# Optimization experiments

Hardware: AMD Instinct MI355X
Metric: run time of the kernel (lower is better)

Reference implementation:

```python
import jax, jax.numpy as jnp
import numpy as np


def setup_inputs() -> dict:
    key = jax.random.key(0)
    ks = jax.random.split(key, 7)
    B, I, H = 8192, 1024, 1024
    x = jax.random.normal(ks[0], (B, I), dtype=jnp.float32)
    h_prev = jax.random.normal(ks[1], (B, H), dtype=jnp.float32)
    C_prev = jax.random.normal(ks[2], (B, H), dtype=jnp.float32)
    W_f = jax.random.normal(ks[3], (I + H, H), dtype=jnp.float32) * 0.01
    W_i = jax.random.normal(ks[4], (I + H, H), dtype=jnp.float32) * 0.01
    W_C = jax.random.normal(ks[5], (I + H, H), dtype=jnp.float32) * 0.01
    W_o = jax.random.normal(ks[6], (I + H, H), dtype=jnp.float32) * 0.01
    b = jnp.zeros((H,), dtype=jnp.float32)
    return {"x": x, "h_prev": h_prev, "C_prev": C_prev,
            "W_f": W_f, "b_f": b, "W_i": W_i, "b_i": b,
            "W_C": W_C, "b_C": b, "W_o": W_o, "b_o": b}


def reference(x, h_prev, C_prev, W_f, b_f, W_i, b_i, W_C, b_C, W_o, b_o):
    combined = jnp.concatenate([x, h_prev], axis=1)  # [B, I+H]
    # Fuse the four gate GEMMs into one [B, I+H] x [I+H, 4H] matmul.
    W = jnp.concatenate([W_f, W_i, W_o, W_C], axis=1)  # [I+H, 4H]
    b = jnp.concatenate([b_f, b_i, b_o, b_C], axis=0)  # [4H]
    gates = combined @ W + b                            # [B, 4H]
    H = C_prev.shape[1]
    f_t = jax.nn.sigmoid(gates[:, 0:H])
    i_t = jax.nn.sigmoid(gates[:, H:2 * H])
    o_t = jax.nn.sigmoid(gates[:, 2 * H:3 * H])
    C_tilda = jnp.tanh(gates[:, 3 * H:4 * H])
    C_t = f_t * C_prev + i_t * C_tilda
    h_t = o_t * jnp.tanh(C_t)
    return (h_t, C_t)
```

## Files before the change

### kernel.cpp

```cpp
#include <hip/hip_runtime.h>
#include <hip/hip_bf16.h>

#define B_SZ 8192
#define IH   2048
#define H_SZ 1024
#define BM   256
#define BK   32
#define NKT  (IH / BK)
#define DB2  32768
#define WOF  16384

typedef __attribute__((ext_vector_type(8))) short  short8;
typedef __attribute__((ext_vector_type(4))) float  floatx4;

static __device__ __forceinline__ ushort f2bf(float f) {
  union { float f; unsigned u; } v; v.f = f;
  unsigned u = v.u;
  u += 0x7fffu + ((u >> 16) & 1u);
  return (ushort)(u >> 16);
}
static __device__ __forceinline__ float sigmoidf_(float x) {
  return 1.0f / (1.0f + __expf(-x));
}
static __device__ __forceinline__ float tanhf_(float x) {
  float ax = fabsf(x);
  float e = __expf(-2.0f * ax);
  float t = (1.0f - e) / (1.0f + e);
  return copysignf(t, x);
}
static __device__ __forceinline__ void gload_lds16(const void* gsrc, void* ldst) {
  __builtin_amdgcn_global_load_lds(
      (__attribute__((address_space(1))) const void*)gsrc,
      (__attribute__((address_space(3))) void*)ldst, 16, 0, 0);
}

__global__ __launch_bounds__(256) void convert_w_kernel(
    const float* __restrict__ Wf, const float* __restrict__ Wi,
    const float* __restrict__ Wo, const float* __restrict__ Wc,
    ushort* __restrict__ Wt) {
  __shared__ float tile[64][65];
  const int g  = blockIdx.z;
  const float* W = (g == 0) ? Wf : (g == 1) ? Wi : (g == 2) ? Wo : Wc;
  const int n0 = blockIdx.x * 64;
  const int k0 = blockIdx.y * 64;
  const int tid = threadIdx.x;
#pragma unroll
  for (int i = 0; i < 4; ++i) {
    int c = i * 256 + tid;
    int r = c >> 4, c4 = c & 15;
    float4 v = *(const float4*)(W + (size_t)(k0 + r) * H_SZ + n0 + c4 * 4);
    tile[r][c4 * 4 + 0] = v.x;
    tile[r][c4 * 4 + 1] = v.y;
    tile[r][c4 * 4 + 2] = v.z;
    tile[r][c4 * 4 + 3] = v.w;
  }
  __syncthreads();
  const int n  = tid >> 2;
  const int kc = (tid & 3) * 16;
  ushort o[16] __attribute__((aligned(16)));
#pragma unroll
  for (int e = 0; e < 16; ++e) o[e] = f2bf(tile[kc + e][n]);
  ushort* dst = Wt + ((size_t)g * H_SZ + n0 + n) * IH + k0 + kc;
  *(uint4*)(dst)     = *(uint4*)&o[0];
  *(uint4*)(dst + 8) = *(uint4*)&o[8];
}

__global__ __launch_bounds__(256) void convert_a_kernel(
    const float* __restrict__ x, const float* __restrict__ hp,
    ushort* __restrict__ Abf) {
  size_t idx = ((size_t)blockIdx.x * 256 + threadIdx.x) * 8;
  size_t row = idx >> 11;
  size_t col = idx & 2047;
  const float* src = (col < 1024) ? (x  + row * 1024 + col)
                                  : (hp + row * 1024 + (col - 1024));
  float4 v0 = *(const float4*)(src);
  float4 v1 = *(const float4*)(src + 4);
  ushort o[8] __attribute__((aligned(16)));
  o[0] = f2bf(v0.x); o[1] = f2bf(v0.y); o[2] = f2bf(v0.z); o[3] = f2bf(v0.w);
  o[4] = f2bf(v1.x); o[5] = f2bf(v1.y); o[6] = f2bf(v1.z); o[7] = f2bf(v1.w);
  *(uint4*)(Abf + idx) = *(uint4*)&o[0];
}

__global__ __launch_bounds__(512, 2) void lstm_fused_kernel(
    const float* __restrict__ Cp, const ushort* __restrict__ Wt,
    const ushort* __restrict__ Abf,
    const float* __restrict__ bf_, const float* __restrict__ bi_,
    const float* __restrict__ bo_, const float* __restrict__ bc_,
    float* __restrict__ out) {
  __shared__ char lds[2 * DB2];

  const int bid = blockIdx.x;
  const int wg  = (bid & 7) * 64 + (bid >> 3);
  const int b0  = (wg >> 4) * BM;
  const int n0g = (wg & 15) * 64;

  const int tid = threadIdx.x;
  const int ln  = tid & 63;
  const int wv  = tid >> 6;
  const int wm  = wv >> 1, wn = wv & 1;

  floatx4 acc[4][8];
#pragma unroll
  for (int m = 0; m < 4; ++m)
#pragma unroll
    for (int j = 0; j < 8; ++j) acc[m][j] = {0.f, 0.f, 0.f, 0.f};

  const int q  = ((ln & 15) >> 1) & 3;
  const int sx = ((ln >> 4) ^ q) << 4;
  const int aB = (wm * 64 + (ln & 15)) * 64 + sx;
  const int bB = WOF + (wn * 32 + (ln & 15)) * 64 + sx;

  const unsigned kg = ((unsigned)(tid & 3)) ^ ((unsigned)(tid >> 3) & 3);
  const char* AbfB = (const char*)Abf;
  const char* WtB  = (const char*)Wt;
  unsigned aoff[2], woff[2];
#pragma unroll
  for (int i = 0; i < 2; ++i) {
    int row = i * 128 + (tid >> 2);
    aoff[i] = (unsigned)(b0 + row) * 4096u + kg * 16u;
    int gate = row >> 6, nloc = row & 63;
    woff[i] = (unsigned)(gate * 1024 + n0g + nloc) * 4096u + kg * 16u;
  }
  const int dst0 = wv * 1024;

#define STAGE(db, ktb)                                                        \
  do {                                                                        \
    gload_lds16(AbfB + (aoff[0] + (unsigned)(ktb)), lds + (db) + dst0);       \
    gload_lds16(AbfB + (aoff[1] + (unsigned)(ktb)), lds + (db) + 8192 + dst0);\
    gload_lds16(WtB  + (woff[0] + (unsigned)(ktb)), lds + (db) + WOF + dst0); \
    gload_lds16(WtB  + (woff[1] + (unsigned)(ktb)), lds + (db) + WOF + 8192 + dst0);\
  } while (0)

  short8 aFA[4], bFA[8];
  short8 aFB[4], bFB[8];
#define RDSET(AF, BF, db)                                                     \
  do {                                                                        \
    _Pragma("unroll")                                                         \
    for (int mf_ = 0; mf_ < 4; ++mf_)                                         \
      AF[mf_] = *(const short8*)(lds + (db) + aB + mf_ * 1024);               \
    _Pragma("unroll")                                                         \
    for (int j_ = 0; j_ < 8; ++j_)                                            \
      BF[j_] = *(const short8*)(lds + (db) + bB + (j_ >> 1) * 4096 +          \
                                (j_ & 1) * 1024);                             \
  } while (0)
#define MFALL(AF, BF)                                                         \
  do {                                                                        \
    __builtin_amdgcn_s_setprio(1);                                            \
    _Pragma("unroll")                                                         \
    for (int mf_ = 0; mf_ < 4; ++mf_)                                         \
      _Pragma("unroll")                                                       \
      for (int j_ = 0; j_ < 8; ++j_)                                          \
        acc[mf_][j_] = __builtin_amdgcn_mfma_f32_16x16x32_bf16(               \
            AF[mf_], BF[j_], acc[mf_][j_], 0, 0, 0);                          \
    __builtin_amdgcn_s_setprio(0);                                            \
  } while (0)
#define BAR    __builtin_amdgcn_s_barrier()
#define LGKM0  asm volatile("s_waitcnt lgkmcnt(0)" ::: "memory")
#define VMC0   asm volatile("s_waitcnt vmcnt(0)" ::: "memory")

  STAGE(0, 0);
  STAGE(DB2, 64);
  VMC0; BAR;
  RDSET(aFA, bFA, 0);
  LGKM0; BAR;

#pragma unroll 1
  for (int it = 0; it < NKT / 2; ++it) {
    {
      const int ktb = (((2 * it + 2) & 63)) * 64;
      RDSET(aFB, bFB, DB2);
      STAGE(0, ktb);
      MFALL(aFA, bFA);
      LGKM0; VMC0; BAR;
    }
    {
      const int ktb = (((2 * it + 3) & 63)) * 64;
      RDSET(aFA, bFA, 0);
      STAGE(DB2, ktb);
      MFALL(aFB, bFB);
      LGKM0; VMC0; BAR;
    }
  }

  const int colq = ln & 15;
  const int rq   = ln >> 4;
  float* outh = out;
  float* outC = out + (size_t)B_SZ * H_SZ;
#pragma unroll
  for (int mf = 0; mf < 4; ++mf) {
#pragma unroll
    for (int ns = 0; ns < 2; ++ns) {
      int n = n0g + wn * 32 + ns * 16 + colq;
      float vbf = bf_[n], vbi = bi_[n], vbo = bo_[n], vbc = bc_[n];
#pragma unroll
      for (int r = 0; r < 4; ++r) {
        int row = b0 + wm * 64 + mf * 16 + rq * 4 + r;
        float fg = sigmoidf_(acc[mf][0 + ns][r] + vbf);
        float ig = sigmoidf_(acc[mf][2 + ns][r] + vbi);
        float og = sigmoidf_(acc[mf][4 + ns][r] + vbo);
        float cg = tanhf_  (acc[mf][6 + ns][r] + vbc);
        float cp = Cp[(size_t)row * H_SZ + n];
        float Ct = fg * cp + ig * cg;
        float ht = og * tanhf_(Ct);
        outh[(size_t)row * H_SZ + n] = ht;
        outC[(size_t)row * H_SZ + n] = Ct;
      }
    }
  }
#undef STAGE
#undef RDSET
#undef MFALL
#undef BAR
#undef LGKM0
#undef VMC0
}

extern "C" void kernel_launch(void* const* d_in, const int* in_sizes, int n_in,
                              void* d_out, int out_size, void* d_ws, size_t ws_size,
                              hipStream_t stream) {
  const float* x  = (const float*)d_in[0];
  const float* hp = (const float*)d_in[1];
  const float* Cp = (const float*)d_in[2];
  const float* Wf = (const float*)d_in[3];
  const float* bf = (const float*)d_in[4];
  const float* Wi = (const float*)d_in[5];
  const float* bi = (const float*)d_in[6];
  const float* Wc = (const float*)d_in[7];
  const float* bc = (const float*)d_in[8];
  const float* Wo = (const float*)d_in[9];
  const float* bo = (const float*)d_in[10];

  ushort* Wt  = (ushort*)d_ws;
  ushort* Abf = (ushort*)((char*)d_ws + (16u << 20));

  dim3 gridT(16, 32, 4);
  convert_w_kernel<<<gridT, 256, 0, stream>>>(Wf, Wi, Wo, Wc, Wt);
  convert_a_kernel<<<8192, 256, 0, stream>>>(x, hp, Abf);

  lstm_fused_kernel<<<512, 512, 0, stream>>>(Cp, Wt, Abf,
                                             bf, bi, bo, bc, (float*)d_out);
}
```

Baseline: 163.8 us.

## Switch to 32x32x16 MFMA with k-major layouts and direct global A-fragment loads

The activation and weight conversion kernels now write k-chunk-major (8-element groups) layouts, so MFMA fragments can be fetched as contiguous 16-byte vectors. The GEMM kernel moves from 16x16x32 to 32x32x16 bf16 MFMA tiles, which cuts the number of LDS fragment reads per flop. A operands are loaded straight from global memory into registers instead of being staged through LDS, which halves LDS usage to weights only. The trade-off is that A-fragment global latency now sits on the critical path with only a single-step register prefetch, and the activation converter gains a tiled transpose pass.

```diff
diff --git a/kernel.cpp b/kernel.cpp
--- a/kernel.cpp
+++ b/kernel.cpp
@@ -7,11 +7,10 @@
 #define BM   256
 #define BK   32
 #define NKT  (IH / BK)
-#define DB2  32768
-#define WOF  16384
-
-typedef __attribute__((ext_vector_type(8))) short  short8;
-typedef __attribute__((ext_vector_type(4))) float  floatx4;
+#define WBUF 16384
+
+typedef __attribute__((ext_vector_type(8)))  short  short8;
+typedef __attribute__((ext_vector_type(16))) float  floatx16;
 
 static __device__ __forceinline__ ushort f2bf(float f) {
   union { float f; unsigned u; } v; v.f = f;
@@ -34,10 +33,10 @@
       (__attribute__((address_space(3))) void*)ldst, 16, 0, 0);
 }
 
-__global__ __launch_bounds__(256) void convert_w_kernel(
+__global__ __launch_bounds__(256) void convert_w2_kernel(
     const float* __restrict__ Wf, const float* __restrict__ Wi,
     const float* __restrict__ Wo, const float* __restrict__ Wc,
-    ushort* __restrict__ Wt) {
+    ushort* __restrict__ Wt2) {
   __shared__ float tile[64][65];
   const int g  = blockIdx.z;
   const float* W = (g == 0) ? Wf : (g == 1) ? Wi : (g == 2) ? Wo : Wc;
@@ -55,39 +54,59 @@
     tile[r][c4 * 4 + 3] = v.w;
   }
   __syncthreads();
-  const int n  = tid >> 2;
-  const int kc = (tid & 3) * 16;
-  ushort o[16] __attribute__((aligned(16)));
-#pragma unroll
-  for (int e = 0; e < 16; ++e) o[e] = f2bf(tile[kc + e][n]);
-  ushort* dst = Wt + ((size_t)g * H_SZ + n0 + n) * IH + k0 + kc;
-  *(uint4*)(dst)     = *(uint4*)&o[0];
-  *(uint4*)(dst + 8) = *(uint4*)&o[8];
-}
-
-__global__ __launch_bounds__(256) void convert_a_kernel(
+#pragma unroll
+  for (int i = 0; i < 2; ++i) {
+    int u  = i * 256 + tid;
+    int kc = u >> 6;
+    int n  = u & 63;
+    ushort o[8] __attribute__((aligned(16)));
+#pragma unroll
+    for (int e = 0; e < 8; ++e) o[e] = f2bf(tile[kc * 8 + e][n]);
+    ushort* dst = Wt2 + (((size_t)(k0 / 8 + kc) * 4 + g) * 1024 + n0 + n) * 8;
+    *(uint4*)dst = *(uint4*)&o[0];
+  }
+}
+
+__global__ __launch_bounds__(256) void convert_a2_kernel(
     const float* __restrict__ x, const float* __restrict__ hp,
-    ushort* __restrict__ Abf) {
-  size_t idx = ((size_t)blockIdx.x * 256 + threadIdx.x) * 8;
-  size_t row = idx >> 11;
-  size_t col = idx & 2047;
-  const float* src = (col < 1024) ? (x  + row * 1024 + col)
-                                  : (hp + row * 1024 + (col - 1024));
-  float4 v0 = *(const float4*)(src);
-  float4 v1 = *(const float4*)(src + 4);
-  ushort o[8] __attribute__((aligned(16)));
-  o[0] = f2bf(v0.x); o[1] = f2bf(v0.y); o[2] = f2bf(v0.z); o[3] = f2bf(v0.w);
-  o[4] = f2bf(v1.x); o[5] = f2bf(v1.y); o[6] = f2bf(v1.z); o[7] = f2bf(v1.w);
-  *(uint4*)(Abf + idx) = *(uint4*)&o[0];
+    ushort* __restrict__ Abf2) {
+  __shared__ float tile[64][65];
+  const int k0 = blockIdx.x * 64;
+  const int r0 = blockIdx.y * 64;
+  const int tid = threadIdx.x;
+  const float* base = (k0 < 1024) ? x : hp;
+  const int koff = (k0 < 1024) ? k0 : (k0 - 1024);
+#pragma unroll
+  for (int i = 0; i < 4; ++i) {
+    int c = i * 256 + tid;
+    int r = c >> 4, c4 = c & 15;
+    float4 v = *(const float4*)(base + (size_t)(r0 + r) * 1024 + koff + c4 * 4);
+    tile[r][c4 * 4 + 0] = v.x;
+    tile[r][c4 * 4 + 1] = v.y;
+    tile[r][c4 * 4 + 2] = v.z;
+    tile[r][c4 * 4 + 3] = v.w;
+  }
+  __syncthreads();
+#pragma unroll
+  for (int i = 0; i < 2; ++i) {
+    int u  = i * 256 + tid;
+    int kc = u >> 6;
+    int r  = u & 63;
+    ushort o[8] __attribute__((aligned(16)));
+#pragma unroll
+    for (int e = 0; e < 8; ++e) o[e] = f2bf(tile[r][kc * 8 + e]);
+    ushort* dst = Abf2 + ((size_t)(k0 / 8 + kc) * 8192 + r0 + r) * 8;
+    *(uint4*)dst = *(uint4*)&o[0];
+  }
 }
 
 __global__ __launch_bounds__(512, 2) void lstm_fused_kernel(
-    const float* __restrict__ Cp, const ushort* __restrict__ Wt,
-    const ushort* __restrict__ Abf,
+    const float* __restrict__ Cp, const ushort* __restrict__ Wt2,
+    const ushort* __restrict__ Abf2,
     const float* __restrict__ bf_, const float* __restrict__ bi_,
     const float* __restrict__ bo_, const float* __restrict__ bc_,
     float* __restrict__ out) {
-  __shared__ char lds[2 * DB2];
+  __shared__ char lds[2 * WBUF];
 
   const int bid = blockIdx.x;
   const int wg  = (bid & 7) * 64 + (bid >> 3);
@@ -99,116 +118,127 @@
   const int wv  = tid >> 6;
   const int wm  = wv >> 1, wn = wv & 1;
 
-  floatx4 acc[4][8];
-#pragma unroll
-  for (int m = 0; m < 4; ++m)
-#pragma unroll
-    for (int j = 0; j < 8; ++j) acc[m][j] = {0.f, 0.f, 0.f, 0.f};
-
-  const int q  = ((ln & 15) >> 1) & 3;
-  const int sx = ((ln >> 4) ^ q) << 4;
-  const int aB = (wm * 64 + (ln & 15)) * 64 + sx;
-  const int bB = WOF + (wn * 32 + (ln & 15)) * 64 + sx;
-
-  const unsigned kg = ((unsigned)(tid & 3)) ^ ((unsigned)(tid >> 3) & 3);
-  const char* AbfB = (const char*)Abf;
-  const char* WtB  = (const char*)Wt;
-  unsigned aoff[2], woff[2];
+  floatx16 acc[2][4];
+#pragma unroll
+  for (int m = 0; m < 2; ++m)
+#pragma unroll
+    for (int j = 0; j < 4; ++j)
+#pragma unroll
+      for (int e = 0; e < 16; ++e) acc[m][j][e] = 0.f;
+
+  const char* Abf2B = (const char*)Abf2;
+  const unsigned aG = (unsigned)(ln >> 5) * 131072u +
+                      (unsigned)(b0 + wm * 64 + (ln & 31)) * 16u;
+
+  const int bRB = (ln >> 5) * 4096 + (wn * 32 + (ln & 31)) * 16;
+
+  const char* WtB = (const char*)Wt2;
+  unsigned wS[2];
 #pragma unroll
   for (int i = 0; i < 2; ++i) {
-    int row = i * 128 + (tid >> 2);
-    aoff[i] = (unsigned)(b0 + row) * 4096u + kg * 16u;
-    int gate = row >> 6, nloc = row & 63;
-    woff[i] = (unsigned)(gate * 1024 + n0g + nloc) * 4096u + kg * 16u;
-  }
-  const int dst0 = wv * 1024;
-
-#define STAGE(db, ktb)                                                        \
-  do {                                                                        \
-    gload_lds16(AbfB + (aoff[0] + (unsigned)(ktb)), lds + (db) + dst0);       \
-    gload_lds16(AbfB + (aoff[1] + (unsigned)(ktb)), lds + (db) + 8192 + dst0);\
-    gload_lds16(WtB  + (woff[0] + (unsigned)(ktb)), lds + (db) + WOF + dst0); \
-    gload_lds16(WtB  + (woff[1] + (unsigned)(ktb)), lds + (db) + WOF + 8192 + dst0);\
-  } while (0)
-
-  short8 aFA[4], bFA[8];
-  short8 aFB[4], bFB[8];
-#define RDSET(AF, BF, db)                                                     \
+    int c    = 2 * i + (tid >> 8);
+    int nrt  = tid & 255;
+    wS[i] = (unsigned)c * 65536u + (unsigned)(nrt >> 6) * 16384u +
+            (unsigned)(n0g + (nrt & 63)) * 16u;
+  }
+  const int wdst0 = wv * 1024;
+
+#define STAGE_W(db, ktw)                                                      \
+  do {                                                                        \
+    gload_lds16(WtB + (wS[0] + (unsigned)(ktw)), lds + (db) + wdst0);         \
+    gload_lds16(WtB + (wS[1] + (unsigned)(ktw)), lds + (db) + 8192 + wdst0);  \
+  } while (0)
+
+  short8 aFA[2][2], aFB[2][2];
+  short8 bFA[4][2], bFB[4][2];
+#define LOADA(AF, kta)                                                        \
   do {                                                                        \
     _Pragma("unroll")                                                         \
-    for (int mf_ = 0; mf_ < 4; ++mf_)                                         \
-      AF[mf_] = *(const short8*)(lds + (db) + aB + mf_ * 1024);               \
+    for (int mt_ = 0; mt_ < 2; ++mt_)                                         \
+      _Pragma("unroll")                                                       \
+      for (int ks_ = 0; ks_ < 2; ++ks_)                                       \
+        AF[mt_][ks_] = *(const short8*)(Abf2B + (aG + (unsigned)(kta) +       \
+                         (unsigned)ks_ * 262144u + (unsigned)mt_ * 512u));    \
+  } while (0)
+#define RDSET_B(BF, db)                                                       \
+  do {                                                                        \
     _Pragma("unroll")                                                         \
-    for (int j_ = 0; j_ < 8; ++j_)                                            \
-      BF[j_] = *(const short8*)(lds + (db) + bB + (j_ >> 1) * 4096 +          \
-                                (j_ & 1) * 1024);                             \
+    for (int g_ = 0; g_ < 4; ++g_)                                            \
+      _Pragma("unroll")                                                       \
+      for (int ks_ = 0; ks_ < 2; ++ks_)                                       \
+        BF[g_][ks_] = *(const short8*)(lds + (db) + bRB + ks_ * 8192 +        \
+                                       g_ * 1024);                            \
   } while (0)
 #define MFALL(AF, BF)                                                         \
   do {                                                                        \
     __builtin_amdgcn_s_setprio(1);                                            \
     _Pragma("unroll")                                                         \
-    for (int mf_ = 0; mf_ < 4; ++mf_)                                         \
+    for (int ks_ = 0; ks_ < 2; ++ks_)                                         \
       _Pragma("unroll")                                                       \
-      for (int j_ = 0; j_ < 8; ++j_)                                          \
-        acc[mf_][j_] = __builtin_amdgcn_mfma_f32_16x16x32_bf16(               \
-            AF[mf_], BF[j_], acc[mf_][j_], 0, 0, 0);                          \
+      for (int mt_ = 0; mt_ < 2; ++mt_)                                       \
+        _Pragma("unroll")                                                     \
+        for (int g_ = 0; g_ < 4; ++g_)                                        \
+          acc[mt_][g_] = __builtin_amdgcn_mfma_f32_32x32x16_bf16(             \
+              AF[mt_][ks_], BF[g_][ks_], acc[mt_][g_], 0, 0, 0);              \
     __builtin_amdgcn_s_setprio(0);                                            \
   } while (0)
 #define BAR    __builtin_amdgcn_s_barrier()
 #define LGKM0  asm volatile("s_waitcnt lgkmcnt(0)" ::: "memory")
 #define VMC0   asm volatile("s_waitcnt vmcnt(0)" ::: "memory")
 
-  STAGE(0, 0);
-  STAGE(DB2, 64);
+  STAGE_W(0, 0);
+  STAGE_W(WBUF, 262144);
+  LOADA(aFA, 0);
   VMC0; BAR;
-  RDSET(aFA, bFA, 0);
+  RDSET_B(bFA, 0);
   LGKM0; BAR;
 
 #pragma unroll 1
   for (int it = 0; it < NKT / 2; ++it) {
     {
-      const int ktb = (((2 * it + 2) & 63)) * 64;
-      RDSET(aFB, bFB, DB2);
-      STAGE(0, ktb);
+      const unsigned ktaN = (unsigned)((2 * it + 1) & 63) * 524288u;
+      const unsigned ktwN = (unsigned)((2 * it + 2) & 63) * 262144u;
+      RDSET_B(bFB, WBUF);
+      LOADA(aFB, ktaN);
+      STAGE_W(0, ktwN);
       MFALL(aFA, bFA);
       LGKM0; VMC0; BAR;
     }
     {
-      const int ktb = (((2 * it + 3) & 63)) * 64;
-      RDSET(aFA, bFA, 0);
-      STAGE(DB2, ktb);
+      const unsigned ktaN = (unsigned)((2 * it + 2) & 63) * 524288u;
+      const unsigned ktwN = (unsigned)((2 * it + 3) & 63) * 262144u;
+      RDSET_B(bFA, 0);
+      LOADA(aFA, ktaN);
+      STAGE_W(WBUF, ktwN);
       MFALL(aFB, bFB);
       LGKM0; VMC0; BAR;
     }
   }
 
-  const int colq = ln & 15;
-  const int rq   = ln >> 4;
+  const int n = n0g + wn * 32 + (ln & 31);
+  const float vbf = bf_[n], vbi = bi_[n], vbo = bo_[n], vbc = bc_[n];
+  const int h2 = (ln >> 5) * 4;
   float* outh = out;
   float* outC = out + (size_t)B_SZ * H_SZ;
 #pragma unroll
-  for (int mf = 0; mf < 4; ++mf) {
-#pragma unroll
-    for (int ns = 0; ns < 2; ++ns) {
-      int n = n0g + wn * 32 + ns * 16 + colq;
-      float vbf = bf_[n], vbi = bi_[n], vbo = bo_[n], vbc = bc_[n];
-#pragma unroll
-      for (int r = 0; r < 4; ++r) {
-        int row = b0 + wm * 64 + mf * 16 + rq * 4 + r;
-        float fg = sigmoidf_(acc[mf][0 + ns][r] + vbf);
-        float ig = sigmoidf_(acc[mf][2 + ns][r] + vbi);
-        float og = sigmoidf_(acc[mf][4 + ns][r] + vbo);
-        float cg = tanhf_  (acc[mf][6 + ns][r] + vbc);
-        float cp = Cp[(size_t)row * H_SZ + n];
-        float Ct = fg * cp + ig * cg;
-        float ht = og * tanhf_(Ct);
-        outh[(size_t)row * H_SZ + n] = ht;
-        outC[(size_t)row * H_SZ + n] = Ct;
-      }
+  for (int mt = 0; mt < 2; ++mt) {
+#pragma unroll
+    for (int reg = 0; reg < 16; ++reg) {
+      int row = b0 + wm * 64 + mt * 32 + (reg & 3) + 8 * (reg >> 2) + h2;
+      float fg = sigmoidf_(acc[mt][0][reg] + vbf);
+      float ig = sigmoidf_(acc[mt][1][reg] + vbi);
+      float og = sigmoidf_(acc[mt][2][reg] + vbo);
+      float cg = tanhf_  (acc[mt][3][reg] + vbc);
+      float cp = Cp[(size_t)row * H_SZ + n];
+      float Ct = fg * cp + ig * cg;
+      float ht = og * tanhf_(Ct);
+      outh[(size_t)row * H_SZ + n] = ht;
+      outC[(size_t)row * H_SZ + n] = Ct;
     }
   }
-#undef STAGE
-#undef RDSET
+#undef STAGE_W
+#undef LOADA
+#undef RDSET_B
 #undef MFALL
 #undef BAR
 #undef LGKM0
@@ -230,13 +260,14 @@
   const float* Wo = (const float*)d_in[9];
   const float* bo = (const float*)d_in[10];
 
-  ushort* Wt  = (ushort*)d_ws;
-  ushort* Abf = (ushort*)((char*)d_ws + (16u << 20));
-
-  dim3 gridT(16, 32, 4);
-  convert_w_kernel<<<gridT, 256, 0, stream>>>(Wf, Wi, Wo, Wc, Wt);
-  convert_a_kernel<<<8192, 256, 0, stream>>>(x, hp, Abf);
-
-  lstm_fused_kernel<<<512, 512, 0, stream>>>(Cp, Wt, Abf,
+  ushort* Wt2  = (ushort*)d_ws;
+  ushort* Abf2 = (ushort*)((char*)d_ws + (16u << 20));
+
+  dim3 gridW(16, 32, 4);
+  convert_w2_kernel<<<gridW, 256, 0, stream>>>(Wf, Wi, Wo, Wc, Wt2);
+  dim3 gridA(32, 128);
+  convert_a2_kernel<<<gridA, 256, 0, stream>>>(x, hp, Abf2);
+
+  lstm_fused_kernel<<<512, 512, 0, stream>>>(Cp, Wt2, Abf2,
                                              bf, bi, bo, bc, (float*)d_out);
 }
```

Measured after the change: 170.5 us. 1.04x slower.
